# Performance work log

Measured on AMD Instinct MI355X. Metric: run time of the kernel, lower is better.

Reference implementation:

```python
import jax, jax.numpy as jnp
import numpy as np

PI = np.pi


def _apply_1q(state, gate, wire, n):
    # state: [B, 2**n] complex64; gate: [2,2] (shared) or [B,2,2] (per-sample)
    # PennyLane convention: wire 0 is the most-significant bit of the state index.
    B = state.shape[0]
    left, right = 2 ** wire, 2 ** (n - wire - 1)
    s = state.reshape(B, left, 2, right)
    if gate.ndim == 2:
        s = jnp.einsum('kl,balr->bakr', gate, s)
    else:
        s = jnp.einsum('bkl,balr->bakr', gate, s)
    return s.reshape(B, -1)


def _apply_cz(state, wire, n):
    # CZ on (wire, wire+1): flip sign of |..11..> amplitudes
    B = state.shape[0]
    left, right = 2 ** wire, 2 ** (n - wire - 2)
    s = state.reshape(B, left, 2, 2, right)
    s = s.at[:, :, 1, 1, :].multiply(-1.0)
    return s.reshape(B, -1)


def _ry_batched(theta):
    # theta: [B] -> [B,2,2] complex RY(theta)
    h = 0.5 * theta
    c, s = jnp.cos(h), jnp.sin(h)
    g = jnp.stack([jnp.stack([c, -s], -1), jnp.stack([s, c], -1)], -2)
    return g.astype(jnp.complex64)


def _rot(phi, theta, omega):
    # Rot = RZ(omega) @ RY(theta) @ RZ(phi)
    c, s = jnp.cos(0.5 * theta), jnp.sin(0.5 * theta)
    e_mm = jnp.exp(-0.5j * (phi + omega))
    e_pm = jnp.exp(0.5j * (phi - omega))
    e_mp = jnp.exp(-0.5j * (phi - omega))
    e_pp = jnp.exp(0.5j * (phi + omega))
    g = jnp.stack([jnp.stack([e_mm * c, -e_pm * s]), jnp.stack([e_mp * s, e_pp * c])])
    return g.astype(jnp.complex64)


def _simulate(enc, weights):
    # enc: [B, n_qubits] in [-1,1]; weights: [n_layers, n_qubits, 3]
    n_layers, n, _ = weights.shape
    B = enc.shape[0]
    state = jnp.zeros((B, 2 ** n), jnp.complex64).at[:, 0].set(1.0)
    ry = [_ry_batched(enc[:, i] * PI) for i in range(n)]
    for l in range(n_layers):
        for i in range(n):
            state = _apply_1q(state, ry[i], i, n)
        for i in range(n):
            state = _apply_1q(state, _rot(weights[l, i, 0], weights[l, i, 1], weights[l, i, 2]), i, n)
        for i in range(n - 1):
            state = _apply_cz(state, i, n)
    for i in range(n):
        state = _apply_1q(state, ry[i], i, n)
    probs = state.real ** 2 + state.imag ** 2  # [B, 2**n]
    # <Z_i> = sum_k probs[k] * (-1)^bit_i(k), wire 0 = MSB
    bits = (jnp.arange(2 ** n)[None, :] >> (n - 1 - jnp.arange(n))[:, None]) & 1
    signs = (1 - 2 * bits).astype(probs.dtype)  # [n, 2**n]
    return probs @ signs.T  # [B, n]


def setup_inputs() -> dict:
    B, D, NQ, NL, NA = 32768, 16, 8, 4, 4
    key = jax.random.key(0)
    ks = jax.random.split(key, 6)

    def lin(k, o, i):
        b = 1.0 / np.sqrt(i)
        k1, k2 = jax.random.split(k)
        return (jax.random.uniform(k1, (o, i), jnp.float32, -b, b),
                jax.random.uniform(k2, (o,), jnp.float32, -b, b))

    enc_w1, enc_b1 = lin(ks[1], 8, D)
    enc_w2, enc_b2 = lin(ks[2], NQ, 8)
    dec_w1, dec_b1 = lin(ks[3], 8, NQ)
    dec_w2, dec_b2 = lin(ks[4], NA, 8)
    q_weights = jax.random.uniform(ks[5], (NL, NQ, 3), jnp.float32, 0.0, 2.0 * PI)
    x = jax.random.normal(ks[0], (B, D), jnp.float32)
    return {"x": x, "enc_w1": enc_w1, "enc_b1": enc_b1, "enc_w2": enc_w2, "enc_b2": enc_b2,
            "q_weights": q_weights, "dec_w1": dec_w1, "dec_b1": dec_b1, "dec_w2": dec_w2, "dec_b2": dec_b2}


def reference(x, enc_w1, enc_b1, enc_w2, enc_b2, q_weights, dec_w1, dec_b1, dec_w2, dec_b2):
    h = jax.nn.relu(x @ enc_w1.T + enc_b1)
    enc = jnp.tanh(h @ enc_w2.T + enc_b2)          # [B, n_qubits]
    q = _simulate(enc, q_weights)                  # [B, n_qubits] PauliZ expvals
    h2 = jax.nn.relu(q @ dec_w1.T + dec_b1)
    return h2 @ dec_w2.T + dec_b2                  # [B, n_actions]
```

## Files before the change

### kernel.cpp

```cpp
#include <hip/hip_runtime.h>
#include <math.h>


#define PI_F 3.14159265358979323846f

struct C2 { float re, im; };

__device__ __forceinline__ C2 cmul(C2 a, C2 b) {
    C2 r;
    r.re = fmaf(a.re, b.re, -a.im * b.im);
    r.im = fmaf(a.re, b.im,  a.im * b.re);
    return r;
}

__device__ __forceinline__ void cdot2(const C2& g, float ar, float ai,
                                      const C2& h, float br, float bi,
                                      float& outr, float& outi) {
    outr = fmaf(g.re, ar, fmaf(-g.im, ai, fmaf(h.re, br, -h.im * bi)));
    outi = fmaf(g.re, ai, fmaf( g.im, ar, fmaf(h.re, bi,  h.im * br)));
}

__device__ __forceinline__ void load_G(const float* __restrict__ c_lds, int g,
                                       float cc, float ss,
                                       C2& G00, C2& G01, C2& G10, C2& G11) {
    const float4* cp = (const float4*)(c_lds + 8 * g);
    float4 c0 = cp[0];
    float4 c1 = cp[1];
    G00.re = fmaf(c0.x, cc,  c0.z * ss);  G00.im = fmaf(c0.y, cc,  c0.w * ss);
    G01.re = fmaf(c0.z, cc, -c0.x * ss);  G01.im = fmaf(c0.w, cc, -c0.y * ss);
    G10.re = fmaf(c1.x, cc,  c1.z * ss);  G10.im = fmaf(c1.y, cc,  c1.w * ss);
    G11.re = fmaf(c1.z, cc, -c1.x * ss);  G11.im = fmaf(c1.w, cc, -c1.y * ss);
}

__device__ __forceinline__ void apply_gate16(int q, int lane,
                                             C2 G00, C2 G01, C2 G10, C2 G11,
                                             float sr[16], float si[16]) {
    if (q < 4) {
        const int sh = 3 - q;
        const int m = 1 << sh;
        const bool hi = (lane >> sh) & 1;
        C2 cS = hi ? G11 : G00;
        C2 cO = hi ? G10 : G01;
#pragma unroll
        for (int t = 0; t < 16; t++) {
            float pr = __shfl_xor(sr[t], m, 64);
            float pi = __shfl_xor(si[t], m, 64);
            float nr, ni;
            cdot2(cS, sr[t], si[t], cO, pr, pi, nr, ni);
            sr[t] = nr; si[t] = ni;
        }
    } else {
        const int st = 1 << (7 - q);
#pragma unroll
        for (int t = 0; t < 16; t++) {
            if ((t & st) == 0) {
                const int u = t + st;
                float ar = sr[t], ai = si[t], br = sr[u], bi = si[u];
                cdot2(G00, ar, ai, G01, br, bi, sr[t], si[t]);
                cdot2(G10, ar, ai, G11, br, bi, sr[u], si[u]);
            }
        }
    }
}

__device__ __constant__ const bool CZNEG[16] =
    { false,false,false,true,  false,false,true,false,
      false,false,false,true,  true, true, false,true };

__global__ __launch_bounds__(256) void qdqn_kernel(
    const float* __restrict__ x,
    const float* __restrict__ ew1, const float* __restrict__ eb1,
    const float* __restrict__ ew2, const float* __restrict__ eb2,
    const float* __restrict__ qw,
    const float* __restrict__ dw1, const float* __restrict__ db1,
    const float* __restrict__ dw2, const float* __restrict__ db2,
    float* __restrict__ out, int B, int NL) {
    __shared__ __align__(16) float c_lds[64 * 8];

    const int tid = threadIdx.x;
    const int n_gates = NL * 8;

    if (tid < n_gates) {
        const int g = tid;
        float phi = qw[3 * g + 0], th = qw[3 * g + 1], om = qw[3 * g + 2];
        float c = __cosf(0.5f * th), s = __sinf(0.5f * th);
        float A = 0.5f * (phi + om), Bb = 0.5f * (phi - om);
        float cA = __cosf(A), sA = __sinf(A), cB = __cosf(Bb), sB = __sinf(Bb);
        float* o = c_lds + 8 * g;
        o[0] =  cA * c;  o[1] = -sA * c;
        o[2] = -cB * s;  o[3] = -sB * s;
        o[4] =  cB * s;  o[5] = -sB * s;
        o[6] =  cA * c;  o[7] =  sA * c;
    }
    __syncthreads();

    const int wave = tid >> 6;
    const int lane = tid & 63;
    const int L = lane & 15;
    int s = (blockIdx.x * 4 + wave) * 4 + (lane >> 4);
    if (s >= B) s = B - 1;

    float xv[16];
    const float4* xp = (const float4*)(x + s * 16);
#pragma unroll
    for (int i = 0; i < 4; i++) {
        float4 v = xp[i];
        xv[4*i] = v.x; xv[4*i+1] = v.y; xv[4*i+2] = v.z; xv[4*i+3] = v.w;
    }
    float hbuf[8];
#pragma unroll
    for (int j = 0; j < 8; j++) {
        float a = eb1[j];
#pragma unroll
        for (int i = 0; i < 16; i++) a = fmaf(ew1[j * 16 + i], xv[i], a);
        hbuf[j] = fmaxf(a, 0.0f);
    }
    float cq[8], sq[8];
#pragma unroll
    for (int q = 0; q < 8; q++) {
        float a = eb2[q];
#pragma unroll
        for (int j = 0; j < 8; j++) a = fmaf(ew2[q * 8 + j], hbuf[j], a);
        float e = 1.0f - __fdividef(2.0f, __expf(2.0f * a) + 1.0f);
        float ang = e * (0.5f * PI_F);
        cq[q] = __cosf(ang);
        sq[q] = __sinf(ang);
    }

    {
    }
    const int L0 = L & 1, L1b = (L >> 1) & 1, L2b = (L >> 2) & 1, L3b = (L >> 3) & 1;
    const int cnt = (L3b & L2b) + (L2b & L1b) + (L1b & L0);
    const float mL = (cnt & 1) ? -1.0f : 1.0f;
    const float mH = L0 ? -mL : mL;

    float sr[16], si[16];
    {
        C2 P; P.re = 1.0f; P.im = 0.0f;
        C2 F[4][2];
#pragma unroll
        for (int q = 0; q < 8; q++) {
            C2 G00, G01, G10, G11;
            load_G(c_lds, q, cq[q], sq[q], G00, G01, G10, G11);
            if (q < 4) {
                const int sh = 3 - q;
                const bool hi = (lane >> sh) & 1;
                C2 f = hi ? G10 : G00;
                P = cmul(P, f);
            } else {
                F[q - 4][0] = G00;
                F[q - 4][1] = G10;
            }
        }
        C2 A0 = cmul(P, F[0][0]), A1 = cmul(P, F[0][1]);
        C2 Bv[4];
        Bv[0] = cmul(A0, F[1][0]); Bv[1] = cmul(A0, F[1][1]);
        Bv[2] = cmul(A1, F[1][0]); Bv[3] = cmul(A1, F[1][1]);
        C2 Cv[8];
#pragma unroll
        for (int i = 0; i < 8; i++) Cv[i] = cmul(Bv[i >> 1], F[2][i & 1]);
#pragma unroll
        for (int t = 0; t < 16; t++) {
            C2 v = cmul(Cv[t >> 1], F[3][t & 1]);
            float m = (t < 8) ? mL : mH;
            m = CZNEG[t] ? -m : m;
            sr[t] = v.re * m;
            si[t] = v.im * m;
        }
    }

    for (int l = 1; l < NL; l++) {
#pragma unroll
        for (int q = 0; q < 8; q++) {
            C2 G00, G01, G10, G11;
            load_G(c_lds, l * 8 + q, cq[q], sq[q], G00, G01, G10, G11);
            apply_gate16(q, lane, G00, G01, G10, G11, sr, si);
        }
#pragma unroll
        for (int t = 0; t < 16; t++) {
            float m = (t < 8) ? mL : mH;
            m = CZNEG[t] ? -m : m;
            sr[t] *= m; si[t] *= m;
        }
    }

#pragma unroll
    for (int q = 0; q < 8; q++) {
        const float c = cq[q], sv = sq[q];
        if (q < 4) {
            const int sh = 3 - q;
            const int m = 1 << sh;
            const bool hi = (lane >> sh) & 1;
            const float cO = hi ? sv : -sv;
#pragma unroll
            for (int t = 0; t < 16; t++) {
                float pr = __shfl_xor(sr[t], m, 64);
                float pi = __shfl_xor(si[t], m, 64);
                sr[t] = fmaf(c, sr[t], cO * pr);
                si[t] = fmaf(c, si[t], cO * pi);
            }
        } else {
            const int st = 1 << (7 - q);
#pragma unroll
            for (int t = 0; t < 16; t++) {
                if ((t & st) == 0) {
                    const int u = t + st;
                    float ar = sr[t], ai = si[t], br = sr[u], bi = si[u];
                    sr[t] = fmaf(c, ar, -sv * br); si[t] = fmaf(c, ai, -sv * bi);
                    sr[u] = fmaf(sv, ar,  c * br); si[u] = fmaf(sv, ai,  c * bi);
                }
            }
        }
    }

    float p[16];
#pragma unroll
    for (int t = 0; t < 16; t++) p[t] = fmaf(sr[t], sr[t], si[t] * si[t]);

    float e0 = p[0]+p[1],  e1 = p[2]+p[3],  e2 = p[4]+p[5],  e3 = p[6]+p[7];
    float e4 = p[8]+p[9],  e5 = p[10]+p[11], e6 = p[12]+p[13], e7 = p[14]+p[15];
    float q0 = e0+e1, q1 = e2+e3, q2 = e4+e5, q3 = e6+e7;
    float h0 = q0+q1, h1 = q2+q3;
    float sumP = h0 + h1;

    float z[8];
#pragma unroll
    for (int w = 0; w < 4; w++)
        z[w] = ((L >> (3 - w)) & 1) ? -sumP : sumP;
    z[4] = h0 - h1;
    z[5] = (q0 - q1) + (q2 - q3);
    z[6] = (e0 - e1) + (e2 - e3) + (e4 - e5) + (e6 - e7);
    z[7] = (p[0]-p[1]) + (p[2]-p[3]) + (p[4]-p[5]) + (p[6]-p[7])
         + (p[8]-p[9]) + (p[10]-p[11]) + (p[12]-p[13]) + (p[14]-p[15]);

#pragma unroll
    for (int m = 1; m < 16; m <<= 1) {
#pragma unroll
        for (int w = 0; w < 8; w++) z[w] += __shfl_xor(z[w], m, 64);
    }

    float h2[8];
#pragma unroll
    for (int j = 0; j < 8; j++) {
        float a = db1[j];
#pragma unroll
        for (int w = 0; w < 8; w++) a = fmaf(dw1[j * 8 + w], z[w], a);
        h2[j] = fmaxf(a, 0.0f);
    }
    if (L < 4) {
        float a = db2[L];
#pragma unroll
        for (int j = 0; j < 8; j++) a = fmaf(dw2[L * 8 + j], h2[j], a);
        out[s * 4 + L] = a;
    }
}

extern "C" void kernel_launch(void* const* d_in, const int* in_sizes, int n_in,
                              void* d_out, int out_size, void* d_ws, size_t ws_size,
                              hipStream_t stream) {
    const float* x   = (const float*)d_in[0];
    const float* ew1 = (const float*)d_in[1];
    const float* eb1 = (const float*)d_in[2];
    const float* ew2 = (const float*)d_in[3];
    const float* eb2 = (const float*)d_in[4];
    const float* qw  = (const float*)d_in[5];
    const float* dw1 = (const float*)d_in[6];
    const float* db1 = (const float*)d_in[7];
    const float* dw2 = (const float*)d_in[8];
    const float* db2 = (const float*)d_in[9];
    float* out = (float*)d_out;

    int B = in_sizes[0] / 16;
    int n_gates = in_sizes[5] / 3;
    int NL = n_gates / 8;

    int blocks = (B + 15) / 16;
    qdqn_kernel<<<blocks, 256, 0, stream>>>(x, ew1, eb1, ew2, eb2, qw,
                                            dw1, db1, dw2, db2, out, B, NL);
}
```

Baseline: 139.0 us.

## Simulate circuit layers with f16 MFMA Kronecker-factored gate products, one sample per wave

Replaces the per-lane register and shuffle statevector update with MFMA matmuls. For each layer it builds fused 4-qubit Kronecker gate matrices in f16 and multiplies them against the 256-amplitude state, one sample per wave. It folds RY encoding into the Rot gates, applies CZ signs as a per-lane mask, and moves the encoder and decoder MLPs to a lane-parallel form through LDS. It also launches four times more blocks. Precision drops to f16 for the state and gates between layers, which risks accuracy, and each wave now handles one sample instead of four.

```diff
diff --git a/kernel.cpp b/kernel.cpp
--- a/kernel.cpp
+++ b/kernel.cpp
@@ -4,8 +4,11 @@
 
 #define PI_F 3.14159265358979323846f
 
+typedef _Float16 f16;
+typedef f16 half8 __attribute__((ext_vector_type(8)));
+typedef float floatx4 __attribute__((ext_vector_type(4)));
+
 struct C2 { float re, im; };
-
 __device__ __forceinline__ C2 cmul(C2 a, C2 b) {
     C2 r;
     r.re = fmaf(a.re, b.re, -a.im * b.im);
@@ -13,59 +16,39 @@
     return r;
 }
 
-__device__ __forceinline__ void cdot2(const C2& g, float ar, float ai,
-                                      const C2& h, float br, float bi,
-                                      float& outr, float& outi) {
-    outr = fmaf(g.re, ar, fmaf(-g.im, ai, fmaf(h.re, br, -h.im * bi)));
-    outi = fmaf(g.re, ai, fmaf( g.im, ar, fmaf(h.re, bi,  h.im * br)));
-}
-
-__device__ __forceinline__ void load_G(const float* __restrict__ c_lds, int g,
-                                       float cc, float ss,
-                                       C2& G00, C2& G01, C2& G10, C2& G11) {
-    const float4* cp = (const float4*)(c_lds + 8 * g);
-    float4 c0 = cp[0];
-    float4 c1 = cp[1];
-    G00.re = fmaf(c0.x, cc,  c0.z * ss);  G00.im = fmaf(c0.y, cc,  c0.w * ss);
-    G01.re = fmaf(c0.z, cc, -c0.x * ss);  G01.im = fmaf(c0.w, cc, -c0.y * ss);
-    G10.re = fmaf(c1.x, cc,  c1.z * ss);  G10.im = fmaf(c1.y, cc,  c1.w * ss);
-    G11.re = fmaf(c1.z, cc, -c1.x * ss);  G11.im = fmaf(c1.w, cc, -c1.y * ss);
-}
-
-__device__ __forceinline__ void apply_gate16(int q, int lane,
-                                             C2 G00, C2 G01, C2 G10, C2 G11,
-                                             float sr[16], float si[16]) {
-    if (q < 4) {
-        const int sh = 3 - q;
-        const int m = 1 << sh;
-        const bool hi = (lane >> sh) & 1;
-        C2 cS = hi ? G11 : G00;
-        C2 cO = hi ? G10 : G01;
-#pragma unroll
-        for (int t = 0; t < 16; t++) {
-            float pr = __shfl_xor(sr[t], m, 64);
-            float pi = __shfl_xor(si[t], m, 64);
-            float nr, ni;
-            cdot2(cS, sr[t], si[t], cO, pr, pi, nr, ni);
-            sr[t] = nr; si[t] = ni;
-        }
-    } else {
-        const int st = 1 << (7 - q);
-#pragma unroll
-        for (int t = 0; t < 16; t++) {
-            if ((t & st) == 0) {
-                const int u = t + st;
-                float ar = sr[t], ai = si[t], br = sr[u], bi = si[u];
-                cdot2(G00, ar, ai, G01, br, bi, sr[t], si[t]);
-                cdot2(G10, ar, ai, G11, br, bi, sr[u], si[u]);
-            }
-        }
-    }
-}
-
-__device__ __constant__ const bool CZNEG[16] =
-    { false,false,false,true,  false,false,true,false,
-      false,false,false,true,  true, true, false,true };
+__device__ __forceinline__ C2 gsel0(float4 g, int i) {
+    C2 r; r.re = i ? g.z : g.x; r.im = i ? g.w : g.y; return r;
+}
+__device__ __forceinline__ C2 gsel1(float4 g, int i) {
+    C2 r; r.re = i ? g.x : -g.z; r.im = i ? -g.y : g.w; return r;
+}
+__device__ __forceinline__ C2 gselrt(float4 g, int i, int j) {
+    C2 a = gsel0(g, i), b = gsel1(g, i);
+    C2 r; r.re = j ? b.re : a.re; r.im = j ? b.im : a.im; return r;
+}
+
+__device__ __forceinline__ void buildB(float4 ga, float4 gb, float4 gc, float4 gd,
+                                       int iA, int iB, int iC, int iD,
+                                       int jA, int jB,
+                                       half8& Bre, half8& Bim) {
+    C2 sA = gselrt(ga, iA, jA);
+    C2 sB = gselrt(gb, iB, jB);
+    C2 P = cmul(sA, sB);
+    C2 c0 = gsel0(gc, iC), c1 = gsel1(gc, iC);
+    C2 d0 = gsel0(gd, iD), d1 = gsel1(gd, iD);
+    C2 E0 = cmul(P, cmul(c0, d0));
+    C2 E1 = cmul(P, cmul(c0, d1));
+    C2 E2 = cmul(P, cmul(c1, d0));
+    C2 E3 = cmul(P, cmul(c1, d1));
+    Bre[0] = (f16)E0.re; Bre[1] = (f16)(-E0.im);
+    Bre[2] = (f16)E1.re; Bre[3] = (f16)(-E1.im);
+    Bre[4] = (f16)E2.re; Bre[5] = (f16)(-E2.im);
+    Bre[6] = (f16)E3.re; Bre[7] = (f16)(-E3.im);
+    Bim[0] = (f16)E0.im; Bim[1] = (f16)E0.re;
+    Bim[2] = (f16)E1.im; Bim[3] = (f16)E1.re;
+    Bim[4] = (f16)E2.im; Bim[5] = (f16)E2.re;
+    Bim[6] = (f16)E3.im; Bim[7] = (f16)E3.re;
+}
 
 __global__ __launch_bounds__(256) void qdqn_kernel(
     const float* __restrict__ x,
@@ -75,183 +58,196 @@
     const float* __restrict__ dw1, const float* __restrict__ db1,
     const float* __restrict__ dw2, const float* __restrict__ db2,
     float* __restrict__ out, int B, int NL) {
-    __shared__ __align__(16) float c_lds[64 * 8];
+    __shared__ __align__(16) float c_lds[32 * 4];
+    __shared__ __align__(16) float gx[4][8][4];
+    __shared__ __align__(16) float hx[4][8];
 
     const int tid = threadIdx.x;
-    const int n_gates = NL * 8;
-
-    if (tid < n_gates) {
-        const int g = tid;
-        float phi = qw[3 * g + 0], th = qw[3 * g + 1], om = qw[3 * g + 2];
-        float c = __cosf(0.5f * th), s = __sinf(0.5f * th);
-        float A = 0.5f * (phi + om), Bb = 0.5f * (phi - om);
-        float cA = __cosf(A), sA = __sinf(A), cB = __cosf(Bb), sB = __sinf(Bb);
-        float* o = c_lds + 8 * g;
-        o[0] =  cA * c;  o[1] = -sA * c;
-        o[2] = -cB * s;  o[3] = -sB * s;
-        o[4] =  cB * s;  o[5] = -sB * s;
-        o[6] =  cA * c;  o[7] =  sA * c;
-    }
-    __syncthreads();
-
     const int wave = tid >> 6;
     const int lane = tid & 63;
     const int L = lane & 15;
-    int s = (blockIdx.x * 4 + wave) * 4 + (lane >> 4);
+    const int q = lane >> 4;
+    int s = blockIdx.x * 4 + wave;
     if (s >= B) s = B - 1;
 
-    float xv[16];
-    const float4* xp = (const float4*)(x + s * 16);
-#pragma unroll
-    for (int i = 0; i < 4; i++) {
-        float4 v = xp[i];
-        xv[4*i] = v.x; xv[4*i+1] = v.y; xv[4*i+2] = v.z; xv[4*i+3] = v.w;
-    }
-    float hbuf[8];
-#pragma unroll
-    for (int j = 0; j < 8; j++) {
-        float a = eb1[j];
-#pragma unroll
-        for (int i = 0; i < 16; i++) a = fmaf(ew1[j * 16 + i], xv[i], a);
-        hbuf[j] = fmaxf(a, 0.0f);
-    }
-    float cq[8], sq[8];
-#pragma unroll
-    for (int q = 0; q < 8; q++) {
-        float a = eb2[q];
-#pragma unroll
-        for (int j = 0; j < 8; j++) a = fmaf(ew2[q * 8 + j], hbuf[j], a);
-        float e = 1.0f - __fdividef(2.0f, __expf(2.0f * a) + 1.0f);
+    const int n_gates = NL * 8;
+    if (tid < n_gates) {
+        const int gg = tid;
+        float phi = qw[3 * gg + 0], th = qw[3 * gg + 1], om = qw[3 * gg + 2];
+        float c = __cosf(0.5f * th), sv = __sinf(0.5f * th);
+        float A = 0.5f * (phi + om), Bb = 0.5f * (phi - om);
+        float* o = c_lds + 4 * gg;
+        o[0] =  __cosf(A) * c;   o[1] = -__sinf(A) * c;
+        o[2] =  __cosf(Bb) * sv; o[3] = -__sinf(Bb) * sv;
+    }
+    __syncthreads();
+
+    float cqv = 1.0f, sqv = 0.0f;
+    {
+        float xv[16];
+        const float4* xp = (const float4*)(x + s * 16);
+#pragma unroll
+        for (int i = 0; i < 4; i++) {
+            float4 v = xp[i];
+            xv[4*i] = v.x; xv[4*i+1] = v.y; xv[4*i+2] = v.z; xv[4*i+3] = v.w;
+        }
+        const int r = lane & 7;
+        float a = eb1[r];
+#pragma unroll
+        for (int i = 0; i < 16; i++) a = fmaf(ew1[r * 16 + i], xv[i], a);
+        if (lane < 8) hx[wave][r] = fmaxf(a, 0.0f);
+        __builtin_amdgcn_wave_barrier();
+        float4 h01 = *(const float4*)&hx[wave][0];
+        float4 h23 = *(const float4*)&hx[wave][4];
+        float b = eb2[r];
+        b = fmaf(ew2[r*8+0], h01.x, b); b = fmaf(ew2[r*8+1], h01.y, b);
+        b = fmaf(ew2[r*8+2], h01.z, b); b = fmaf(ew2[r*8+3], h01.w, b);
+        b = fmaf(ew2[r*8+4], h23.x, b); b = fmaf(ew2[r*8+5], h23.y, b);
+        b = fmaf(ew2[r*8+6], h23.z, b); b = fmaf(ew2[r*8+7], h23.w, b);
+        float e = 1.0f - __fdividef(2.0f, __expf(2.0f * b) + 1.0f);
         float ang = e * (0.5f * PI_F);
-        cq[q] = __cosf(ang);
-        sq[q] = __sinf(ang);
+        cqv = __cosf(ang);
+        sqv = __sinf(ang);
+    }
+
+    const int L0 = L & 1, L1b = (L >> 1) & 1, L2b = (L >> 2) & 1, L3b = (L >> 3) & 1;
+    const int c3 = (q >> 1) & 1, c2 = q & 1;
+    const int pr = (L3b & L2b) ^ (L2b & L1b) ^ (L1b & L0);
+    const int cross = L0 & c3;
+    float czs[4];
+#pragma unroll
+    for (int u = 0; u < 4; u++) {
+        int c1 = (u >> 1) & 1, c0 = u & 1;
+        int pc = (c3 & c2) ^ (c2 & c1) ^ (c1 & c0);
+        czs[u] = ((pr ^ cross ^ pc) & 1) ? -1.0f : 1.0f;
+    }
+
+    const int iA = L3b, iB = L2b, iC = L1b, iD = L0;
+    const int jA = c3, jB = c2;
+
+    half8 A;
+    floatx4 dre, dim;
+    const floatx4 zf = {0.0f, 0.0f, 0.0f, 0.0f};
+
+    for (int l = 0; l <= NL; l++) {
+        if (lane < 8) {
+            float ar, ai, br, bi;
+            if (l < NL) {
+                const float4 c0 = *(const float4*)(c_lds + 4 * (l * 8 + lane));
+                ar = fmaf(c0.x, cqv, -c0.z * sqv);
+                ai = fmaf(c0.y, cqv,  c0.w * sqv);
+                br = fmaf(c0.z, cqv,  c0.x * sqv);
+                bi = fmaf(c0.w, cqv, -c0.y * sqv);
+            } else {
+                ar = cqv; ai = 0.0f; br = sqv; bi = 0.0f;
+            }
+            *(float4*)gx[wave][lane] = make_float4(ar, ai, br, bi);
+        }
+        __builtin_amdgcn_wave_barrier();
+
+        if (l == 0) {
+            float4 g0 = *(const float4*)gx[wave][0];
+            float4 g1 = *(const float4*)gx[wave][1];
+            float4 g2 = *(const float4*)gx[wave][2];
+            float4 g3 = *(const float4*)gx[wave][3];
+            float4 g4 = *(const float4*)gx[wave][4];
+            float4 g5 = *(const float4*)gx[wave][5];
+            float4 g6 = *(const float4*)gx[wave][6];
+            float4 g7 = *(const float4*)gx[wave][7];
+            C2 Pr = cmul(cmul(gsel0(g0, iA), gsel0(g1, iB)),
+                         cmul(gsel0(g2, iC), gsel0(g3, iD)));
+            C2 Pc = cmul(gsel0(g4, jA), gsel0(g5, jB));
+            C2 P = cmul(Pr, Pc);
+            C2 t60 = gsel0(g6, 0), t61 = gsel0(g6, 1);
+            C2 t70 = gsel0(g7, 0), t71 = gsel0(g7, 1);
+            C2 T[4] = { cmul(t60, t70), cmul(t60, t71),
+                        cmul(t61, t70), cmul(t61, t71) };
+#pragma unroll
+            for (int u = 0; u < 4; u++) {
+                C2 E = cmul(P, T[u]);
+                A[2*u]   = (f16)(E.re * czs[u]);
+                A[2*u+1] = (f16)(E.im * czs[u]);
+            }
+            continue;
+        }
+
+        {
+            float4 g4 = *(const float4*)gx[wave][4];
+            float4 g5 = *(const float4*)gx[wave][5];
+            float4 g6 = *(const float4*)gx[wave][6];
+            float4 g7 = *(const float4*)gx[wave][7];
+            half8 Bre, Bim;
+            buildB(g4, g5, g6, g7, iA, iB, iC, iD, jA, jB, Bre, Bim);
+            dre = __builtin_amdgcn_mfma_f32_16x16x32_f16(A, Bre, zf, 0, 0, 0);
+            dim = __builtin_amdgcn_mfma_f32_16x16x32_f16(A, Bim, zf, 0, 0, 0);
+#pragma unroll
+            for (int u = 0; u < 4; u++) {
+                A[2*u]   = (f16)dre[u];
+                A[2*u+1] = (f16)dim[u];
+            }
+        }
+        {
+            float4 g0 = *(const float4*)gx[wave][0];
+            float4 g1 = *(const float4*)gx[wave][1];
+            float4 g2 = *(const float4*)gx[wave][2];
+            float4 g3 = *(const float4*)gx[wave][3];
+            half8 Bre, Bim;
+            buildB(g0, g1, g2, g3, iA, iB, iC, iD, jA, jB, Bre, Bim);
+            dre = __builtin_amdgcn_mfma_f32_16x16x32_f16(A, Bre, zf, 0, 0, 0);
+            dim = __builtin_amdgcn_mfma_f32_16x16x32_f16(A, Bim, zf, 0, 0, 0);
+            if (l < NL) {
+#pragma unroll
+                for (int u = 0; u < 4; u++) { dre[u] *= czs[u]; dim[u] *= czs[u]; }
+            }
+            if (l < NL) {
+#pragma unroll
+                for (int u = 0; u < 4; u++) {
+                    A[2*u]   = (f16)dre[u];
+                    A[2*u+1] = (f16)dim[u];
+                }
+            }
+        }
+    }
+
+    float p0 = fmaf(dre[0], dre[0], dim[0] * dim[0]);
+    float p1 = fmaf(dre[1], dre[1], dim[1] * dim[1]);
+    float p2 = fmaf(dre[2], dre[2], dim[2] * dim[2]);
+    float p3 = fmaf(dre[3], dre[3], dim[3] * dim[3]);
+    float sumP = (p0 + p1) + (p2 + p3);
+
+    float zW[8];
+    zW[0] = L3b ? -sumP : sumP;
+    zW[1] = L2b ? -sumP : sumP;
+    zW[2] = L1b ? -sumP : sumP;
+    zW[3] = L0  ? -sumP : sumP;
+    zW[4] = c3  ? -sumP : sumP;
+    zW[5] = c2  ? -sumP : sumP;
+    zW[6] = (p0 + p1) - (p2 + p3);
+    zW[7] = (p0 - p1) + (p2 - p3);
+
+#pragma unroll
+    for (int m = 1; m < 64; m <<= 1) {
+#pragma unroll
+        for (int w = 0; w < 8; w++) zW[w] += __shfl_xor(zW[w], m, 64);
     }
 
     {
-    }
-    const int L0 = L & 1, L1b = (L >> 1) & 1, L2b = (L >> 2) & 1, L3b = (L >> 3) & 1;
-    const int cnt = (L3b & L2b) + (L2b & L1b) + (L1b & L0);
-    const float mL = (cnt & 1) ? -1.0f : 1.0f;
-    const float mH = L0 ? -mL : mL;
-
-    float sr[16], si[16];
-    {
-        C2 P; P.re = 1.0f; P.im = 0.0f;
-        C2 F[4][2];
-#pragma unroll
-        for (int q = 0; q < 8; q++) {
-            C2 G00, G01, G10, G11;
-            load_G(c_lds, q, cq[q], sq[q], G00, G01, G10, G11);
-            if (q < 4) {
-                const int sh = 3 - q;
-                const bool hi = (lane >> sh) & 1;
-                C2 f = hi ? G10 : G00;
-                P = cmul(P, f);
-            } else {
-                F[q - 4][0] = G00;
-                F[q - 4][1] = G10;
-            }
-        }
-        C2 A0 = cmul(P, F[0][0]), A1 = cmul(P, F[0][1]);
-        C2 Bv[4];
-        Bv[0] = cmul(A0, F[1][0]); Bv[1] = cmul(A0, F[1][1]);
-        Bv[2] = cmul(A1, F[1][0]); Bv[3] = cmul(A1, F[1][1]);
-        C2 Cv[8];
-#pragma unroll
-        for (int i = 0; i < 8; i++) Cv[i] = cmul(Bv[i >> 1], F[2][i & 1]);
-#pragma unroll
-        for (int t = 0; t < 16; t++) {
-            C2 v = cmul(Cv[t >> 1], F[3][t & 1]);
-            float m = (t < 8) ? mL : mH;
-            m = CZNEG[t] ? -m : m;
-            sr[t] = v.re * m;
-            si[t] = v.im * m;
-        }
-    }
-
-    for (int l = 1; l < NL; l++) {
-#pragma unroll
-        for (int q = 0; q < 8; q++) {
-            C2 G00, G01, G10, G11;
-            load_G(c_lds, l * 8 + q, cq[q], sq[q], G00, G01, G10, G11);
-            apply_gate16(q, lane, G00, G01, G10, G11, sr, si);
-        }
-#pragma unroll
-        for (int t = 0; t < 16; t++) {
-            float m = (t < 8) ? mL : mH;
-            m = CZNEG[t] ? -m : m;
-            sr[t] *= m; si[t] *= m;
-        }
-    }
-
-#pragma unroll
-    for (int q = 0; q < 8; q++) {
-        const float c = cq[q], sv = sq[q];
-        if (q < 4) {
-            const int sh = 3 - q;
-            const int m = 1 << sh;
-            const bool hi = (lane >> sh) & 1;
-            const float cO = hi ? sv : -sv;
-#pragma unroll
-            for (int t = 0; t < 16; t++) {
-                float pr = __shfl_xor(sr[t], m, 64);
-                float pi = __shfl_xor(si[t], m, 64);
-                sr[t] = fmaf(c, sr[t], cO * pr);
-                si[t] = fmaf(c, si[t], cO * pi);
-            }
-        } else {
-            const int st = 1 << (7 - q);
-#pragma unroll
-            for (int t = 0; t < 16; t++) {
-                if ((t & st) == 0) {
-                    const int u = t + st;
-                    float ar = sr[t], ai = si[t], br = sr[u], bi = si[u];
-                    sr[t] = fmaf(c, ar, -sv * br); si[t] = fmaf(c, ai, -sv * bi);
-                    sr[u] = fmaf(sv, ar,  c * br); si[u] = fmaf(sv, ai,  c * bi);
-                }
-            }
-        }
-    }
-
-    float p[16];
-#pragma unroll
-    for (int t = 0; t < 16; t++) p[t] = fmaf(sr[t], sr[t], si[t] * si[t]);
-
-    float e0 = p[0]+p[1],  e1 = p[2]+p[3],  e2 = p[4]+p[5],  e3 = p[6]+p[7];
-    float e4 = p[8]+p[9],  e5 = p[10]+p[11], e6 = p[12]+p[13], e7 = p[14]+p[15];
-    float q0 = e0+e1, q1 = e2+e3, q2 = e4+e5, q3 = e6+e7;
-    float h0 = q0+q1, h1 = q2+q3;
-    float sumP = h0 + h1;
-
-    float z[8];
-#pragma unroll
-    for (int w = 0; w < 4; w++)
-        z[w] = ((L >> (3 - w)) & 1) ? -sumP : sumP;
-    z[4] = h0 - h1;
-    z[5] = (q0 - q1) + (q2 - q3);
-    z[6] = (e0 - e1) + (e2 - e3) + (e4 - e5) + (e6 - e7);
-    z[7] = (p[0]-p[1]) + (p[2]-p[3]) + (p[4]-p[5]) + (p[6]-p[7])
-         + (p[8]-p[9]) + (p[10]-p[11]) + (p[12]-p[13]) + (p[14]-p[15]);
-
-#pragma unroll
-    for (int m = 1; m < 16; m <<= 1) {
-#pragma unroll
-        for (int w = 0; w < 8; w++) z[w] += __shfl_xor(z[w], m, 64);
-    }
-
-    float h2[8];
-#pragma unroll
-    for (int j = 0; j < 8; j++) {
-        float a = db1[j];
-#pragma unroll
-        for (int w = 0; w < 8; w++) a = fmaf(dw1[j * 8 + w], z[w], a);
-        h2[j] = fmaxf(a, 0.0f);
-    }
-    if (L < 4) {
-        float a = db2[L];
-#pragma unroll
-        for (int j = 0; j < 8; j++) a = fmaf(dw2[L * 8 + j], h2[j], a);
-        out[s * 4 + L] = a;
+        const int r = lane & 7;
+        float a = db1[r];
+#pragma unroll
+        for (int w = 0; w < 8; w++) a = fmaf(dw1[r * 8 + w], zW[w], a);
+        if (lane < 8) hx[wave][r] = fmaxf(a, 0.0f);
+        __builtin_amdgcn_wave_barrier();
+        if (lane < 4) {
+            float4 h01 = *(const float4*)&hx[wave][0];
+            float4 h23 = *(const float4*)&hx[wave][4];
+            float acc = db2[lane];
+            acc = fmaf(dw2[lane*8+0], h01.x, acc); acc = fmaf(dw2[lane*8+1], h01.y, acc);
+            acc = fmaf(dw2[lane*8+2], h01.z, acc); acc = fmaf(dw2[lane*8+3], h01.w, acc);
+            acc = fmaf(dw2[lane*8+4], h23.x, acc); acc = fmaf(dw2[lane*8+5], h23.y, acc);
+            acc = fmaf(dw2[lane*8+6], h23.z, acc); acc = fmaf(dw2[lane*8+7], h23.w, acc);
+            out[s * 4 + lane] = acc;
+        }
     }
 }
 
@@ -274,7 +270,7 @@
     int n_gates = in_sizes[5] / 3;
     int NL = n_gates / 8;
 
-    int blocks = (B + 15) / 16;
+    int blocks = (B + 3) / 4;
     qdqn_kernel<<<blocks, 256, 0, stream>>>(x, ew1, eb1, ew2, eb2, qw,
                                             dw1, db1, dw2, db2, out, B, NL);
 }
```

Result: faster. 123.5 us (-11.1%).
